# Kernel tuning notes

Hardware: AMD Instinct MI355X
Metric: run time of the kernel (lower is better)

## Reference

```python
import jax, jax.numpy as jnp
import numpy as np

H = 16       # num_heads
HD = 64      # head_dim = embed_dim // num_heads
CLIP = 64    # clipping_threshold (Shaw et al. k)
B, L, D = 4, 1024, 1024


def setup_inputs() -> dict:
    key = jax.random.key(0)
    ks = jax.random.split(key, 13)
    f = lambda k_, s: jax.random.normal(k_, s, dtype=jnp.float32) * 0.02
    return {
        "q": f(ks[0], (B, L, D)),
        "k": f(ks[1], (B, L, D)),
        "v": f(ks[2], (B, L, D)),
        "Wq": f(ks[3], (D, D)), "bq": jnp.zeros((D,), jnp.float32),
        "Wk": f(ks[4], (D, D)), "bk": jnp.zeros((D,), jnp.float32),
        "Wv": f(ks[5], (D, D)), "bv": jnp.zeros((D,), jnp.float32),
        "Wo": f(ks[6], (D, D)), "bo": jnp.zeros((D,), jnp.float32),
        "Ek": f(ks[7], (2 * CLIP + 1, HD)),  # relative_position_k table
        "Ev": f(ks[8], (2 * CLIP + 1, HD)),  # relative_position_v table
    }


def reference(q, k, v, Wq, bq, Wk, bk, Wv, bv, Wo, bo, Ek, Ev):
    b, lq, d = q.shape
    lk = k.shape[1]
    # input projections (torch Linear: x @ W^T + b)
    qp = (q @ Wq.T + bq).reshape(b, lq, H, HD)
    kp = (k @ Wk.T + bk).reshape(b, lk, H, HD)
    vp = (v @ Wv.T + bv).reshape(b, lk, H, HD)
    # content-content scores
    attn1 = jnp.einsum("bqhd,bkhd->bhqk", qp, kp)
    # relative position embeddings R: (lq, lk, HD)
    idx = jnp.clip(jnp.arange(lk)[None, :] - jnp.arange(lq)[:, None], -CLIP, CLIP) + CLIP
    rel_k = Ek[idx]
    rel_v = Ev[idx]
    # content-position scores (Shaw et al. term added to QK^T)
    attn2 = jnp.einsum("bqhd,qkd->bhqk", qp, rel_k)
    scale = jnp.sqrt(jnp.asarray(HD, dtype=q.dtype))
    attn = jax.nn.softmax((attn1 + attn2) / scale, axis=-1)  # (b,H,lq,lk)
    # weighted values + relative value term
    out1 = jnp.einsum("bhqk,bkhd->bqhd", attn, vp)
    out2 = jnp.einsum("bhqk,qkd->bqhd", attn, rel_v)
    out = (out1 + out2).reshape(b, lq, d)
    return out @ Wo.T + bo
```

## Files before the change

### kernel.cpp

```cpp
#include <hip/hip_runtime.h>
#include <hip/hip_bf16.h>
#include <stdint.h>
#include <stddef.h>

#define B_ 4
#define L_ 1024
#define D_ 1024
#define H_ 16
#define HD_ 64
#define NROW 65536
#define QE_LD 132
#define EV_LD 192
#define T_STR 200

typedef __attribute__((ext_vector_type(8))) short bf16x8;
typedef __attribute__((ext_vector_type(4))) float f32x4;
typedef __attribute__((ext_vector_type(4))) unsigned short u16x4;

__device__ __forceinline__ float bf2f(unsigned short u) {
  union { unsigned int i; float f; } v; v.i = ((unsigned int)u) << 16; return v.f;
}
__device__ __forceinline__ unsigned short f2bf(float f) {
  union { float f; unsigned int i; } v; v.f = f;
  return (unsigned short)((v.i + 0x7fffu + ((v.i >> 16) & 1u)) >> 16);
}
__device__ __forceinline__ unsigned short f2bfrn(float f) {
  __hip_bfloat16 h = __float2bfloat16(f);
  return *reinterpret_cast<unsigned short*>(&h);
}
__device__ __forceinline__ void async16(const void* g, void* l) {
  __builtin_amdgcn_global_load_lds(
      (const __attribute__((address_space(1))) unsigned int*)g,
      (__attribute__((address_space(3))) unsigned int*)l, 16, 0, 0);
}

struct ConvArgs7 { const float* s[7]; unsigned short* d[7]; int n4[7]; };

__global__ __launch_bounds__(256) void f32_to_bf16_multi(ConvArgs7 a) {
  const int y = blockIdx.y;
  const float* s = a.s[y];
  unsigned short* d = a.d[y];
  const int n4 = a.n4[y];
  int i = blockIdx.x * 256 + threadIdx.x;
  int stride = gridDim.x * 256;
  for (; i < n4; i += stride) {
    float4 v = ((const float4*)s)[i];
    u16x4 o;
    o[0] = f2bf(v.x); o[1] = f2bf(v.y); o[2] = f2bf(v.z); o[3] = f2bf(v.w);
    ((u16x4*)d)[i] = o;
  }
}

__global__ __launch_bounds__(256) void build_ekev_k(const float* __restrict__ Ek,
                                                    const float* __restrict__ Ev,
                                                    unsigned short* __restrict__ Ekp,
                                                    unsigned short* __restrict__ EvTp) {
  int i = blockIdx.x * 256 + threadIdx.x;
  if (i < 256 * 64) {
    int r = i >> 6, dd = i & 63;
    Ekp[i] = (r < 129) ? f2bf(Ek[r * 64 + dd]) : (unsigned short)0;
  }
  if (i < 128 * EV_LD) {
    int dd = i / EV_LD, r = i - dd * EV_LD;
    EvTp[i] = (dd < 64 && r < 129) ? f2bf(Ev[r * 64 + dd]) : (unsigned short)0;
  }
}

struct Gemm3 {
  const unsigned short* A[3];
  const unsigned short* Bt[3];
  const float* bias[3];
  void* C[3];
};

template<int MI, bool OBF16, bool BIAS, bool VPT>
__global__ __launch_bounds__(256, 8 / MI) void gemm_bt(Gemm3 ga, int lda, int ldb, int ldc,
                                                       int Ncut, int ktiles) {
  constexpr int BM = MI * 32;
  __shared__ unsigned short Al[2][BM * 32];
  __shared__ unsigned short Bl[2][128 * 32];
  const unsigned short* A = ga.A[blockIdx.z];
  const unsigned short* Bt = ga.Bt[blockIdx.z];
  const float* bias = ga.bias[blockIdx.z];
  void* Cv = ga.C[blockIdx.z];
  const int tid = threadIdx.x;
  const int w = tid >> 6, l = tid & 63;
  const int l15 = l & 15, lg = l >> 4;
  const int row0 = blockIdx.x * BM, col0 = blockIdx.y * 128;
  const int wm = (w >> 1) * (MI * 16), wn = (w & 1) * 64;

  f32x4 acc[MI][4];
#pragma unroll
  for (int i = 0; i < MI; ++i)
#pragma unroll
    for (int j = 0; j < 4; ++j) acc[i][j] = {0.f, 0.f, 0.f, 0.f};

  auto stage = [&](int buf, int kt) {
#pragma unroll
    for (int i = 0; i < MI / 2; ++i) {
      int p = (i * 4 + w) * 1024 + l * 16;
      int m = p >> 6;
      int clog = (l & 3) ^ ((m >> 1) & 3);
      async16(A + (size_t)(row0 + m) * lda + kt * 32 + clog * 8,
              (char*)&Al[buf][0] + (i * 4 + w) * 1024);
    }
#pragma unroll
    for (int i = 0; i < 2; ++i) {
      int p = (i * 4 + w) * 1024 + l * 16;
      int m = p >> 6;
      int clog = (l & 3) ^ ((m >> 1) & 3);
      async16(Bt + (size_t)(col0 + m) * ldb + kt * 32 + clog * 8,
              (char*)&Bl[buf][0] + (i * 4 + w) * 1024);
    }
  };

  stage(0, 0);
  __syncthreads();
  for (int kt = 0; kt < ktiles; ++kt) {
    int cur = kt & 1;
    if (kt + 1 < ktiles) stage(cur ^ 1, kt + 1);
    bf16x8 af[MI], bfr[4];
#pragma unroll
    for (int mi = 0; mi < MI; ++mi) {
      int m = wm + mi * 16 + l15;
      af[mi] = *(const bf16x8*)&Al[cur][m * 32 + ((lg ^ ((m >> 1) & 3)) << 3)];
    }
#pragma unroll
    for (int ni = 0; ni < 4; ++ni) {
      int n = wn + ni * 16 + l15;
      bfr[ni] = *(const bf16x8*)&Bl[cur][n * 32 + ((lg ^ ((n >> 1) & 3)) << 3)];
    }
#pragma unroll
    for (int mi = 0; mi < MI; ++mi)
#pragma unroll
      for (int ni = 0; ni < 4; ++ni)
        acc[mi][ni] = __builtin_amdgcn_mfma_f32_16x16x32_bf16(af[mi], bfr[ni], acc[mi][ni], 0, 0, 0);
    __syncthreads();
  }

  if (VPT && blockIdx.z == 2) {
    unsigned short* vpT = (unsigned short*)Cv;
#pragma unroll
    for (int ni = 0; ni < 4; ++ni) {
      int col = col0 + wn + ni * 16 + l15;
      float bv = BIAS ? bias[col] : 0.f;
#pragma unroll
      for (int mi = 0; mi < MI; ++mi) {
        int rowb = row0 + wm + mi * 16 + lg * 4;
        int bb = rowb >> 10, lrow = rowb & 1023;
        u16x4 o;
#pragma unroll
        for (int r = 0; r < 4; ++r) o[r] = f2bf(acc[mi][ni][r] + bv);
        *(u16x4*)(vpT + ((size_t)((bb * H_ + (col >> 6)) * HD_ + (col & 63))) * L_ + lrow) = o;
      }
    }
    return;
  }

#pragma unroll
  for (int ni = 0; ni < 4; ++ni) {
    int col = col0 + wn + ni * 16 + l15;
    if (col < Ncut) {
      float bv = BIAS ? bias[col] : 0.f;
#pragma unroll
      for (int mi = 0; mi < MI; ++mi) {
        int rowb = row0 + wm + mi * 16 + lg * 4;
#pragma unroll
        for (int r = 0; r < 4; ++r) {
          float v = acc[mi][ni][r] + bv;
          size_t off = (size_t)(rowb + r) * ldc + col;
          if (OBF16) ((unsigned short*)Cv)[off] = f2bf(v);
          else       ((float*)Cv)[off] = v;
        }
      }
    }
  }
}

__global__ __launch_bounds__(256, 4) void flash_fwd_k(
    const unsigned short* __restrict__ qp, const unsigned short* __restrict__ kp,
    const unsigned short* __restrict__ vpT, const unsigned short* __restrict__ qE,
    const unsigned short* __restrict__ EvTp, unsigned short* __restrict__ tmp) {
  __shared__ __align__(16) char smem[32768];
  unsigned short (*Kl)[4096] = (unsigned short (*)[4096])smem;
  unsigned short (*Vl)[4096] = (unsigned short (*)[4096])(smem + 16384);
  const int tid = threadIdx.x, w = tid >> 6, l = tid & 63;
  const int l15 = l & 15, lg = l >> 4;
  const int bid = blockIdx.x;
  const int bh = bid & 63, qt = bid >> 6;
  const int b = bh >> 4, h = bh & 15;
  const int qw = qt * 64 + w * 16;
  const int q_lane = qw + l15;
  const int rowbase = (b * L_ + qw) * H_ + h;
  const int rowi_lane = rowbase + l15 * H_;
  constexpr float C1 = 0.125f * 1.44269504f;

  bf16x8 qf[2];
  {
    const unsigned short* qrp = qp + (size_t)rowi_lane * HD_;
#pragma unroll
    for (int ks = 0; ks < 2; ++ks) qf[ks] = *(const bf16x8*)(qrp + ks * 32 + lg * 8);
  }
  const unsigned short* qerow = qE + (size_t)rowi_lane * QE_LD;
  const float qe0L = bf2f(qerow[0]) * C1;
  const float qe128L = bf2f(qerow[128]) * C1;

  f32x4 O[4];
#pragma unroll
  for (int nd = 0; nd < 4; ++nd) O[nd] = {0.f, 0.f, 0.f, 0.f};
  float mrow = -1e30f, lrow = 0.f, t0row = 0.f;

  u16x4 pks0[4], pks1[4], pks2[4];
  float mu0 = -1e30f, mu1 = -1e30f, mu2 = -1e30f;
  {
    u16x4 z4 = {0, 0, 0, 0};
#pragma unroll
    for (int ni = 0; ni < 4; ++ni) { pks0[ni] = z4; pks1[ni] = z4; pks2[ni] = z4; }
  }

  auto stage = [&](int buf, int kt) {
#pragma unroll
    for (int i = 0; i < 2; ++i) {
      int p = (i * 4 + w) * 1024 + l * 16;
      int row = p >> 7;
      int clog = (l & 7) ^ (row & 7);
      async16(kp + ((size_t)((b * L_ + kt * 64 + row) * H_ + h)) * HD_ + clog * 8,
              (char*)&Kl[buf][0] + (i * 4 + w) * 1024);
      async16(vpT + ((size_t)((b * H_ + h) * HD_ + row)) * L_ + kt * 64 + clog * 8,
              (char*)&Vl[buf][0] + (i * 4 + w) * 1024);
    }
  };

  stage(0, 0);
  __syncthreads();

  for (int kt = 0; kt < 16; ++kt) {
    int cur = kt & 1;
    if (kt + 1 < 16) stage(cur ^ 1, kt + 1);

    f32x4 S[4];
#pragma unroll
    for (int ni = 0; ni < 4; ++ni) S[ni] = {0.f, 0.f, 0.f, 0.f};
#pragma unroll
    for (int ks = 0; ks < 2; ++ks) {
      bf16x8 kf[4];
#pragma unroll
      for (int ni = 0; ni < 4; ++ni) {
        int kk = ni * 16 + l15;
        kf[ni] = *(const bf16x8*)&Kl[cur][kk * 64 + (((ks * 4 + lg) ^ (kk & 7)) << 3)];
      }
#pragma unroll
      for (int ni = 0; ni < 4; ++ni)
        S[ni] = __builtin_amdgcn_mfma_f32_16x16x32_bf16(kf[ni], qf[ks], S[ni], 0, 0, 0);
    }

    const int cls = (kt <= qt - 2) ? 0 : ((kt >= qt + 2) ? 2 : 1);
    const int based = kt * 64 - q_lane;

    if (cls == 1) {
#pragma unroll
      for (int ni = 0; ni < 4; ++ni)
#pragma unroll
        for (int r = 0; r < 4; ++r) {
          int delta = based + ni * 16 + lg * 4 + r;
          int idx = min(max(delta, -64), 64) + 64;
          S[ni][r] = S[ni][r] * C1 + bf2f(qerow[idx]) * C1;
        }
    } else {
      float qeL = (cls == 0) ? qe0L : qe128L;
#pragma unroll
      for (int ni = 0; ni < 4; ++ni)
#pragma unroll
        for (int r = 0; r < 4; ++r) S[ni][r] = S[ni][r] * C1 + qeL;
    }

    float x0 = fmaxf(fmaxf(S[0][0], S[0][1]), fmaxf(S[0][2], S[0][3]));
    float x1 = fmaxf(fmaxf(S[1][0], S[1][1]), fmaxf(S[1][2], S[1][3]));
    float x2 = fmaxf(fmaxf(S[2][0], S[2][1]), fmaxf(S[2][2], S[2][3]));
    float x3 = fmaxf(fmaxf(S[3][0], S[3][1]), fmaxf(S[3][2], S[3][3]));
    float pmax = fmaxf(fmaxf(x0, x1), fmaxf(x2, x3));
    pmax = fmaxf(pmax, __shfl_xor(pmax, 16));
    pmax = fmaxf(pmax, __shfl_xor(pmax, 32));

    float a = 1.f;
    if (!__all(pmax <= mrow + 11.54f)) {
      float mnew = fmaxf(mrow, pmax);
      a = __builtin_amdgcn_exp2f(mrow - mnew);
      mrow = mnew;
      float aq0 = __shfl(a, lg * 4 + 0);
      float aq1 = __shfl(a, lg * 4 + 1);
      float aq2 = __shfl(a, lg * 4 + 2);
      float aq3 = __shfl(a, lg * 4 + 3);
#pragma unroll
      for (int nd = 0; nd < 4; ++nd) {
        O[nd][0] *= aq0; O[nd][1] *= aq1; O[nd][2] *= aq2; O[nd][3] *= aq3;
      }
    }

#pragma unroll
    for (int ni = 0; ni < 4; ++ni)
#pragma unroll
      for (int r = 0; r < 4; ++r)
        S[ni][r] = __builtin_amdgcn_exp2f(S[ni][r] - mrow);

    float s0 = (S[0][0] + S[0][1]) + (S[0][2] + S[0][3]);
    float s1 = (S[1][0] + S[1][1]) + (S[1][2] + S[1][3]);
    float s2 = (S[2][0] + S[2][1]) + (S[2][2] + S[2][3]);
    float s3 = (S[3][0] + S[3][1]) + (S[3][2] + S[3][3]);
    float ps = (s0 + s1) + (s2 + s3);
    ps += __shfl_xor(ps, 16);
    ps += __shfl_xor(ps, 32);
    lrow = lrow * a + ps;

    if (cls == 0) {
      t0row = t0row * a + ps;
    } else if (cls == 2) {
      t0row = t0row * a;
    } else if (kt == qt - 1) {
      float p0 = 0.f;
#pragma unroll
      for (int ni = 0; ni < 4; ++ni)
#pragma unroll
        for (int r = 0; r < 4; ++r)
          if (based + ni * 16 + lg * 4 + r <= -64) p0 += S[ni][r];
      p0 += __shfl_xor(p0, 16);
      p0 += __shfl_xor(p0, 32);
      t0row = t0row * a + p0;
    } else {
      t0row = t0row * a;
    }

    asm volatile("" ::: "memory");
    __builtin_amdgcn_s_barrier();
    asm volatile("" ::: "memory");
    unsigned short* Plw = (unsigned short*)(smem + cur * 8192) + w * 1024;

    u16x4 pcur[4];
#pragma unroll
    for (int ni = 0; ni < 4; ++ni) {
      u16x4 pk;
#pragma unroll
      for (int r = 0; r < 4; ++r) pk[r] = f2bfrn(S[ni][r]);
      pcur[ni] = pk;
      int slot = (ni * 2 + (lg >> 1)) ^ (l15 & 7);
      int addr = l15 * 64 + (slot << 3) + (lg & 1) * 4;
      *(u16x4*)&Plw[addr] = pk;
    }
    if (cls == 1) {
      if (kt == qt - 1) {
#pragma unroll
        for (int ni = 0; ni < 4; ++ni) pks0[ni] = pcur[ni];
        mu0 = mrow;
      } else if (kt == qt) {
#pragma unroll
        for (int ni = 0; ni < 4; ++ni) pks1[ni] = pcur[ni];
        mu1 = mrow;
      } else {
#pragma unroll
        for (int ni = 0; ni < 4; ++ni) pks2[ni] = pcur[ni];
        mu2 = mrow;
      }
    }

#pragma unroll
    for (int ks = 0; ks < 2; ++ks) {
      bf16x8 pf = *(const bf16x8*)&Plw[l15 * 64 + (((ks * 4 + lg) ^ (l15 & 7)) << 3)];
      bf16x8 vf[4];
#pragma unroll
      for (int nd = 0; nd < 4; ++nd) {
        int d = nd * 16 + l15;
        vf[nd] = *(const bf16x8*)&Vl[cur][d * 64 + (((ks * 4 + lg) ^ (d & 7)) << 3)];
      }
#pragma unroll
      for (int nd = 0; nd < 4; ++nd)
        O[nd] = __builtin_amdgcn_mfma_f32_16x16x32_bf16(pf, vf[nd], O[nd], 0, 0, 0);
    }
    __syncthreads();
  }

  unsigned short* Tl16 = (unsigned short*)smem + w * (16 * T_STR);
  {
    u16x4 z4 = {0, 0, 0, 0};
    u16x4* tl4 = (u16x4*)Tl16;
    for (int i = l; i < 16 * T_STR / 4; i += 64) tl4[i] = z4;
  }
  float bandsum = 0.f;
  auto addband = [&](const u16x4* pk, float muv, int btc) {
    float scale = __builtin_amdgcn_exp2f(muv - mrow);
    int jbase = (qt + btc - 1) * 64 + lg * 4 - q_lane + 64;
#pragma unroll
    for (int ni = 0; ni < 4; ++ni)
#pragma unroll
      for (int r = 0; r < 4; ++r) {
        int j = jbase + ni * 16 + r;
        if (j >= 1 && j <= 127) {
          float pf = bf2f((unsigned short)pk[ni][r]) * scale;
          Tl16[l15 * T_STR + j] = f2bfrn(pf);
          bandsum += pf;
        }
      }
  };
  addband(pks0, mu0, 0);
  addband(pks1, mu1, 1);
  addband(pks2, mu2, 2);
  bandsum += __shfl_xor(bandsum, 16);
  bandsum += __shfl_xor(bandsum, 32);
  if (lg == 0) {
    Tl16[l15 * T_STR] = f2bfrn(t0row);
    Tl16[l15 * T_STR + 128] = f2bfrn(fmaxf(0.f, lrow - t0row - bandsum));
  }
#pragma unroll
  for (int ks6 = 0; ks6 < 6; ++ks6) {
    bf16x8 af = *(const bf16x8*)(Tl16 + l15 * T_STR + ks6 * 32 + lg * 8);
    bf16x8 bfr[4];
#pragma unroll
    for (int nd = 0; nd < 4; ++nd)
      bfr[nd] = *(const bf16x8*)(EvTp + (size_t)(nd * 16 + l15) * EV_LD + ks6 * 32 + lg * 8);
#pragma unroll
    for (int nd = 0; nd < 4; ++nd)
      O[nd] = __builtin_amdgcn_mfma_f32_16x16x32_bf16(af, bfr[nd], O[nd], 0, 0, 0);
  }

  float invl = 1.f / lrow;
  float iq[4];
#pragma unroll
  for (int r = 0; r < 4; ++r) iq[r] = __shfl(invl, lg * 4 + r);
#pragma unroll
  for (int r = 0; r < 4; ++r) {
    size_t rowi = (size_t)(rowbase + (lg * 4 + r) * H_);
#pragma unroll
    for (int nd = 0; nd < 4; ++nd)
      tmp[rowi * HD_ + nd * 16 + l15] = f2bfrn(O[nd][r] * iq[r]);
  }
}

extern "C" void kernel_launch(void* const* d_in, const int* in_sizes, int n_in,
                              void* d_out, int out_size, void* d_ws, size_t ws_size,
                              hipStream_t stream) {
  (void)in_sizes; (void)n_in; (void)out_size; (void)ws_size;
  const float* q  = (const float*)d_in[0];
  const float* k  = (const float*)d_in[1];
  const float* v  = (const float*)d_in[2];
  const float* Wq = (const float*)d_in[3];
  const float* bq = (const float*)d_in[4];
  const float* Wk = (const float*)d_in[5];
  const float* bk = (const float*)d_in[6];
  const float* Wv = (const float*)d_in[7];
  const float* bv = (const float*)d_in[8];
  const float* Wo = (const float*)d_in[9];
  const float* bo = (const float*)d_in[10];
  const float* Ek = (const float*)d_in[11];
  const float* Ev = (const float*)d_in[12];

  char* ws = (char*)d_ws;
  constexpr size_t SZ_QKV = (size_t)B_ * L_ * D_ * 2;
  constexpr size_t SZ_W   = (size_t)D_ * D_ * 2;
  constexpr size_t OFF_QB = 0;
  constexpr size_t OFF_KB = OFF_QB + SZ_QKV;
  constexpr size_t OFF_VB = OFF_KB + SZ_QKV;
  constexpr size_t OFF_WQ = OFF_VB + SZ_QKV;
  constexpr size_t OFF_WK = OFF_WQ + SZ_W;
  constexpr size_t OFF_WV = OFF_WK + SZ_W;
  constexpr size_t OFF_WO = OFF_WV + SZ_W;
  constexpr size_t OFF_EKP = OFF_WO + SZ_W;
  constexpr size_t OFF_EVT = OFF_EKP + 256 * 64 * 2;
  constexpr size_t OFF_QE = OFF_EVT + 128 * EV_LD * 2;
  constexpr size_t OFF_QP = OFF_QE + (size_t)NROW * QE_LD * 2;
  constexpr size_t OFF_KP = OFF_QP + SZ_QKV;
  constexpr size_t OFF_VPT = OFF_KP + SZ_QKV;
  constexpr size_t OFF_TMP = OFF_VPT + SZ_QKV;

  auto U16 = [&](size_t off) { return (unsigned short*)(ws + off); };

  {
    ConvArgs7 c{};
    c.s[0] = q;  c.d[0] = U16(OFF_QB); c.n4[0] = (B_ * L_ * D_) / 4;
    c.s[1] = k;  c.d[1] = U16(OFF_KB); c.n4[1] = (B_ * L_ * D_) / 4;
    c.s[2] = v;  c.d[2] = U16(OFF_VB); c.n4[2] = (B_ * L_ * D_) / 4;
    c.s[3] = Wq; c.d[3] = U16(OFF_WQ); c.n4[3] = (D_ * D_) / 4;
    c.s[4] = Wk; c.d[4] = U16(OFF_WK); c.n4[4] = (D_ * D_) / 4;
    c.s[5] = Wv; c.d[5] = U16(OFF_WV); c.n4[5] = (D_ * D_) / 4;
    c.s[6] = Wo; c.d[6] = U16(OFF_WO); c.n4[6] = (D_ * D_) / 4;
    f32_to_bf16_multi<<<dim3(1024, 7), 256, 0, stream>>>(c);
  }
  build_ekev_k<<<96, 256, 0, stream>>>(Ek, Ev, U16(OFF_EKP), U16(OFF_EVT));

  {
    Gemm3 g{};
    g.A[0] = U16(OFF_QB); g.Bt[0] = U16(OFF_WQ); g.bias[0] = bq; g.C[0] = U16(OFF_QP);
    g.A[1] = U16(OFF_KB); g.Bt[1] = U16(OFF_WK); g.bias[1] = bk; g.C[1] = U16(OFF_KP);
    g.A[2] = U16(OFF_VB); g.Bt[2] = U16(OFF_WV); g.bias[2] = bv; g.C[2] = U16(OFF_VPT);
    gemm_bt<4, true, true, true><<<dim3(32, 8, 3), 256, 0, stream>>>(
        g, 1024, 1024, 1024, 1024, 32);
  }

  {
    Gemm3 g{};
    g.A[0] = U16(OFF_QP); g.Bt[0] = U16(OFF_EKP); g.bias[0] = nullptr; g.C[0] = U16(OFF_QE);
    gemm_bt<2, true, false, false><<<dim3(1024, 2, 1), 256, 0, stream>>>(
        g, 64, 64, QE_LD, 129, 2);
  }

  flash_fwd_k<<<1024, 256, 0, stream>>>(
      U16(OFF_QP), U16(OFF_KP), U16(OFF_VPT), U16(OFF_QE), U16(OFF_EVT), U16(OFF_TMP));

  {
    Gemm3 g{};
    g.A[0] = U16(OFF_TMP); g.Bt[0] = U16(OFF_WO); g.bias[0] = bo; g.C[0] = d_out;
    gemm_bt<2, false, true, false><<<dim3(64, 8, 1), 256, 0, stream>>>(
        g, 1024, 1024, 1024, 1024, 32);
  }
}
```

Before: 138.5 us.

## Fold Ek/Ev conversion into cast kernel, trim qE GEMM, add MFMA priority hints

Merges the relative-embedding table conversion into the multi-tensor bf16 cast launch as an extra grid row, removing one kernel launch. The q·Ek GEMM now computes only 128 columns, halving its grid. The missing column-128 term is recomputed in the attention kernel as a per-row dot product. The P staging buffer moves to a dedicated LDS region, which drops a per-tile barrier but raises LDS use and lowers the occupancy hint from 4 to 3 blocks. s_setprio hints are wrapped around the MFMA groups.

```diff
diff --git a/kernel.cpp b/kernel.cpp
--- a/kernel.cpp
+++ b/kernel.cpp
@@ -34,10 +34,26 @@
       (__attribute__((address_space(3))) unsigned int*)l, 16, 0, 0);
 }
 
-struct ConvArgs7 { const float* s[7]; unsigned short* d[7]; int n4[7]; };
-
-__global__ __launch_bounds__(256) void f32_to_bf16_multi(ConvArgs7 a) {
+struct ConvArgs {
+  const float* s[7]; unsigned short* d[7]; int n4[7];
+  const float* ek; const float* ev;
+  unsigned short* ekp; unsigned short* evtp;
+};
+
+__global__ __launch_bounds__(256) void f32_to_bf16_multi(ConvArgs a) {
   const int y = blockIdx.y;
+  if (y == 7) {
+    int i = blockIdx.x * 256 + threadIdx.x;
+    if (i < 256 * 64) {
+      int r = i >> 6, dd = i & 63;
+      a.ekp[i] = (r < 129) ? f2bf(a.ek[r * 64 + dd]) : (unsigned short)0;
+    }
+    if (i < 128 * EV_LD) {
+      int dd = i / EV_LD, r = i - dd * EV_LD;
+      a.evtp[i] = (dd < 64 && r < 129) ? f2bf(a.ev[r * 64 + dd]) : (unsigned short)0;
+    }
+    return;
+  }
   const float* s = a.s[y];
   unsigned short* d = a.d[y];
   const int n4 = a.n4[y];
@@ -48,21 +64,6 @@
     u16x4 o;
     o[0] = f2bf(v.x); o[1] = f2bf(v.y); o[2] = f2bf(v.z); o[3] = f2bf(v.w);
     ((u16x4*)d)[i] = o;
-  }
-}
-
-__global__ __launch_bounds__(256) void build_ekev_k(const float* __restrict__ Ek,
-                                                    const float* __restrict__ Ev,
-                                                    unsigned short* __restrict__ Ekp,
-                                                    unsigned short* __restrict__ EvTp) {
-  int i = blockIdx.x * 256 + threadIdx.x;
-  if (i < 256 * 64) {
-    int r = i >> 6, dd = i & 63;
-    Ekp[i] = (r < 129) ? f2bf(Ek[r * 64 + dd]) : (unsigned short)0;
-  }
-  if (i < 128 * EV_LD) {
-    int dd = i / EV_LD, r = i - dd * EV_LD;
-    EvTp[i] = (dd < 64 && r < 129) ? f2bf(Ev[r * 64 + dd]) : (unsigned short)0;
   }
 }
 
@@ -177,14 +178,16 @@
   }
 }
 
-__global__ __launch_bounds__(256, 4) void flash_fwd_k(
+__global__ __launch_bounds__(256, 3) void flash_fwd_k(
     const unsigned short* __restrict__ qp, const unsigned short* __restrict__ kp,
     const unsigned short* __restrict__ vpT, const unsigned short* __restrict__ qE,
-    const unsigned short* __restrict__ EvTp, unsigned short* __restrict__ tmp) {
-  __shared__ __align__(16) char smem[32768];
+    const unsigned short* __restrict__ Ekp, const unsigned short* __restrict__ EvTp,
+    unsigned short* __restrict__ tmp) {
+  __shared__ __align__(16) char smem[40960];
   unsigned short (*Kl)[4096] = (unsigned short (*)[4096])smem;
   unsigned short (*Vl)[4096] = (unsigned short (*)[4096])(smem + 16384);
   const int tid = threadIdx.x, w = tid >> 6, l = tid & 63;
+  unsigned short* Plw = (unsigned short*)(smem + 32768) + w * 1024;
   const int l15 = l & 15, lg = l >> 4;
   const int bid = blockIdx.x;
   const int bh = bid & 63, qt = bid >> 6;
@@ -203,7 +206,21 @@
   }
   const unsigned short* qerow = qE + (size_t)rowi_lane * QE_LD;
   const float qe0L = bf2f(qerow[0]) * C1;
-  const float qe128L = bf2f(qerow[128]) * C1;
+  float qe128L;
+  {
+    const unsigned short* ek128 = Ekp + 128 * 64;
+    float dot = 0.f;
+#pragma unroll
+    for (int ks = 0; ks < 2; ++ks) {
+      const unsigned short* ep = ek128 + ks * 32 + lg * 8;
+#pragma unroll
+      for (int e = 0; e < 8; ++e)
+        dot += bf2f((unsigned short)qf[ks][e]) * bf2f(ep[e]);
+    }
+    dot += __shfl_xor(dot, 16);
+    dot += __shfl_xor(dot, 32);
+    qe128L = dot * C1;
+  }
 
   f32x4 O[4];
 #pragma unroll
@@ -249,9 +266,11 @@
         int kk = ni * 16 + l15;
         kf[ni] = *(const bf16x8*)&Kl[cur][kk * 64 + (((ks * 4 + lg) ^ (kk & 7)) << 3)];
       }
+      __builtin_amdgcn_s_setprio(1);
 #pragma unroll
       for (int ni = 0; ni < 4; ++ni)
         S[ni] = __builtin_amdgcn_mfma_f32_16x16x32_bf16(kf[ni], qf[ks], S[ni], 0, 0, 0);
+      __builtin_amdgcn_s_setprio(0);
     }
 
     const int cls = (kt <= qt - 2) ? 0 : ((kt >= qt + 2) ? 2 : 1);
@@ -263,8 +282,10 @@
 #pragma unroll
         for (int r = 0; r < 4; ++r) {
           int delta = based + ni * 16 + lg * 4 + r;
-          int idx = min(max(delta, -64), 64) + 64;
-          S[ni][r] = S[ni][r] * C1 + bf2f(qerow[idx]) * C1;
+          float qes;
+          if (delta >= 64) qes = qe128L;
+          else qes = bf2f(qerow[max(delta, -64) + 64]) * C1;
+          S[ni][r] = S[ni][r] * C1 + qes;
         }
     } else {
       float qeL = (cls == 0) ? qe0L : qe128L;
@@ -330,11 +351,6 @@
       t0row = t0row * a;
     }
 
-    asm volatile("" ::: "memory");
-    __builtin_amdgcn_s_barrier();
-    asm volatile("" ::: "memory");
-    unsigned short* Plw = (unsigned short*)(smem + cur * 8192) + w * 1024;
-
     u16x4 pcur[4];
 #pragma unroll
     for (int ni = 0; ni < 4; ++ni) {
@@ -371,9 +387,11 @@
         int d = nd * 16 + l15;
         vf[nd] = *(const bf16x8*)&Vl[cur][d * 64 + (((ks * 4 + lg) ^ (d & 7)) << 3)];
       }
+      __builtin_amdgcn_s_setprio(1);
 #pragma unroll
       for (int nd = 0; nd < 4; ++nd)
         O[nd] = __builtin_amdgcn_mfma_f32_16x16x32_bf16(pf, vf[nd], O[nd], 0, 0, 0);
+      __builtin_amdgcn_s_setprio(0);
     }
     __syncthreads();
   }
@@ -473,7 +491,7 @@
   auto U16 = [&](size_t off) { return (unsigned short*)(ws + off); };
 
   {
-    ConvArgs7 c{};
+    ConvArgs c{};
     c.s[0] = q;  c.d[0] = U16(OFF_QB); c.n4[0] = (B_ * L_ * D_) / 4;
     c.s[1] = k;  c.d[1] = U16(OFF_KB); c.n4[1] = (B_ * L_ * D_) / 4;
     c.s[2] = v;  c.d[2] = U16(OFF_VB); c.n4[2] = (B_ * L_ * D_) / 4;
@@ -481,9 +499,9 @@
     c.s[4] = Wk; c.d[4] = U16(OFF_WK); c.n4[4] = (D_ * D_) / 4;
     c.s[5] = Wv; c.d[5] = U16(OFF_WV); c.n4[5] = (D_ * D_) / 4;
     c.s[6] = Wo; c.d[6] = U16(OFF_WO); c.n4[6] = (D_ * D_) / 4;
-    f32_to_bf16_multi<<<dim3(1024, 7), 256, 0, stream>>>(c);
-  }
-  build_ekev_k<<<96, 256, 0, stream>>>(Ek, Ev, U16(OFF_EKP), U16(OFF_EVT));
+    c.ek = Ek; c.ev = Ev; c.ekp = U16(OFF_EKP); c.evtp = U16(OFF_EVT);
+    f32_to_bf16_multi<<<dim3(1024, 8), 256, 0, stream>>>(c);
+  }
 
   {
     Gemm3 g{};
@@ -497,12 +515,13 @@
   {
     Gemm3 g{};
     g.A[0] = U16(OFF_QP); g.Bt[0] = U16(OFF_EKP); g.bias[0] = nullptr; g.C[0] = U16(OFF_QE);
-    gemm_bt<2, true, false, false><<<dim3(1024, 2, 1), 256, 0, stream>>>(
-        g, 64, 64, QE_LD, 129, 2);
+    gemm_bt<2, true, false, false><<<dim3(1024, 1, 1), 256, 0, stream>>>(
+        g, 64, 64, QE_LD, 128, 2);
   }
 
   flash_fwd_k<<<1024, 256, 0, stream>>>(
-      U16(OFF_QP), U16(OFF_KP), U16(OFF_VPT), U16(OFF_QE), U16(OFF_EVT), U16(OFF_TMP));
+      U16(OFF_QP), U16(OFF_KP), U16(OFF_VPT), U16(OFF_QE),
+      U16(OFF_EKP), U16(OFF_EVT), U16(OFF_TMP));
 
   {
     Gemm3 g{};
```

New measurement: 157.6 us. +13.8%, slower.
